# Kernel tuning notes

Measured on AMD Instinct MI355X. Metric: run time of the kernel, lower is better.

Reference implementation:

```python
import jax, jax.numpy as jnp
import numpy as np

INPUT_DIM = 1024
HIDDEN = 1024
NUM_EXPERTS = 64
TOP_K = 8
N_TOKENS = 32768


def _linear_params(key, fan_in, fan_out):
    kw, kb = jax.random.split(key)
    bound = 1.0 / np.sqrt(fan_in)
    w = jax.random.uniform(kw, (fan_in, fan_out), jnp.float32, -bound, bound)
    b = jax.random.uniform(kb, (fan_out,), jnp.float32, -bound, bound)
    return w, b


def setup_inputs() -> dict:
    key = jax.random.key(0)
    ks = jax.random.split(key, 8)
    x = jax.random.normal(ks[0], (N_TOKENS, INPUT_DIM), jnp.float32)
    noise = jax.random.normal(ks[1], (N_TOKENS, NUM_EXPERTS), jnp.float32)
    h2 = 2 * HIDDEN
    w1, b1 = _linear_params(ks[2], INPUT_DIM, h2)
    w2, b2 = _linear_params(ks[3], h2, h2)
    wn, bn = _linear_params(ks[4], h2, h2)
    w3, b3 = _linear_params(ks[5], h2, HIDDEN)
    w4, b4 = _linear_params(ks[6], HIDDEN, NUM_EXPERTS)
    wz, bz = _linear_params(ks[7], INPUT_DIM, NUM_EXPERTS)
    return {"x": x, "noise": noise, "w1": w1, "b1": b1, "w2": w2, "b2": b2,
            "wn": wn, "bn": bn, "w3": w3, "b3": b3, "w4": w4, "b4": b4,
            "wz": wz, "bz": bz}


def reference(x, noise, w1, b1, w2, b2, wn, bn, w3, b3, w4, b4, wz, bz):
    relu = jax.nn.relu
    h = relu(x @ w1 + b1)            # [N, 2H]
    h = relu(h @ w2 + b2)            # [N, 2H]
    h = relu(h @ wn + bn)            # [N, 2H]
    h = relu(h @ w3 + b3)            # [N, H]
    logits = h @ w4 + b4             # [N, E]
    noise_logits = x @ wz + bz       # [N, E]
    noisy_logits = logits + noise * jax.nn.softplus(noise_logits)
    top_k_logits, indices = jax.lax.top_k(noisy_logits, TOP_K)  # [N, K]
    rows = jnp.arange(noisy_logits.shape[0])[:, None]
    sparse_logits = jnp.full_like(noisy_logits, -jnp.inf).at[rows, indices].set(top_k_logits)
    router_output = jax.nn.softmax(sparse_logits, axis=-1)      # [N, E]
    return router_output, indices
```

## Files before the change

### kernel.cpp

```cpp
#include <hip/hip_runtime.h>
#include <math.h>

#define IN_DIM 1024
#define H2     2048
#define HID    1024
#define NEXP   64
#define TOPK   8
#define RISK_TH 1.5e-4f

typedef short  v8s __attribute__((ext_vector_type(8)));
typedef float  v4f __attribute__((ext_vector_type(4)));

__device__ __forceinline__ void bf16_split(float f, ushort& h, ushort& l) {
    unsigned uh = __float_as_uint(f) & 0xffff0000u;
    h = (ushort)(uh >> 16);
    float r = f - __uint_as_float(uh);
    l = (ushort)(__float_as_uint(r) >> 16);
}

__device__ __forceinline__ void gload16(const ushort* g, ushort* l) {
    __builtin_amdgcn_global_load_lds(
        (const __attribute__((address_space(1))) void*)g,
        (__attribute__((address_space(3))) void*)l, 16, 0, 0);
}

__global__ __launch_bounds__(256)
void split_w_kernel(const float* __restrict__ W, ushort* __restrict__ hiT,
                    ushort* __restrict__ loT, int K, int N)
{
    __shared__ float T[64][65];
    const int k0 = blockIdx.y * 64, n0 = blockIdx.x * 64;
    const int t = threadIdx.x;
#pragma unroll
    for (int j = 0; j < 4; ++j) {
        int idx = t + j * 256;
        int row = idx >> 4;
        int c4  = (idx & 15) * 4;
        float4 f = *(const float4*)(W + (long)(k0 + row) * N + n0 + c4);
        T[row][c4 + 0] = f.x; T[row][c4 + 1] = f.y;
        T[row][c4 + 2] = f.z; T[row][c4 + 3] = f.w;
    }
    __syncthreads();
#pragma unroll
    for (int j = 0; j < 4; ++j) {
        int idx = t + j * 256;
        int nn = idx >> 4;
        int kq = (idx & 15) * 4;
        ushort4 h4, l4;
        bf16_split(T[kq + 0][nn], h4.x, l4.x);
        bf16_split(T[kq + 1][nn], h4.y, l4.y);
        bf16_split(T[kq + 2][nn], h4.z, l4.z);
        bf16_split(T[kq + 3][nn], h4.w, l4.w);
        long o = (long)(n0 + nn) * K + k0 + kq;
        *(ushort4*)(hiT + o) = h4;
        *(ushort4*)(loT + o) = l4;
    }
}

__global__ __launch_bounds__(256)
void split_x_kernel(const float* __restrict__ X, ushort* __restrict__ hi,
                    ushort* __restrict__ lo)
{
    long i = ((long)blockIdx.x * 256 + threadIdx.x) * 4;
    float4 f = *(const float4*)(X + i);
    ushort4 h4, l4;
    bf16_split(f.x, h4.x, l4.x);
    bf16_split(f.y, h4.y, l4.y);
    bf16_split(f.z, h4.z, l4.z);
    bf16_split(f.w, h4.w, l4.w);
    *(ushort4*)(hi + i) = h4;
    *(ushort4*)(lo + i) = l4;
}

template<int MI, int NWN>
__global__ __launch_bounds__(512, 2)
void gemm8p_kernel(const ushort* __restrict__ gAhi, const ushort* __restrict__ gAlo,
                   const ushort* __restrict__ gBhi, const ushort* __restrict__ gBlo,
                   const float* __restrict__ bias,
                   float* __restrict__ Cf32, ushort* __restrict__ Chi,
                   ushort* __restrict__ Clo, int N, int K)
{
    static_assert(MI == 2 * NWN, "wave grid must tile 256 rows");
    constexpr int BN    = NWN * 64;
    constexpr int ATILE = 256 * 32;
    constexpr int BTILE = BN * 32;
    constexpr int BUFU  = 2 * ATILE + 2 * BTILE;
    constexpr int MH    = MI / 2;
    __shared__ __align__(16) ushort lds[2 * BUFU];

    const int tid  = threadIdx.x;
    const int w    = tid >> 6;
    const int lane = tid & 63;
    const int wm   = w / NWN;
    const int wn   = w % NWN;
    const int q    = lane >> 4;
    const int l15  = lane & 15;

    const int nwg = (int)(gridDim.x * gridDim.y);
    const int h   = (int)(blockIdx.y * gridDim.x + blockIdx.x);
    const int l   = (h & 7) * (nwg >> 3) + (h >> 3);
    const long bm = (long)(l >> 3) * 256;
    const long bn = (long)(l & 7) * BN;

    const int  e   = lane >> 2;
    const int  s8  = (((lane & 3) ^ ((lane >> 3) & 3)) * 8);
    const int  fragUS = ((q ^ ((l15 >> 1) & 3)) * 8);

    const int NT = K >> 5;

    v4f acc[MI][4];
#pragma unroll
    for (int mi = 0; mi < MI; ++mi)
#pragma unroll
        for (int ni = 0; ni < 4; ++ni)
            acc[mi][ni] = (v4f){0.f, 0.f, 0.f, 0.f};

    {
        ushort* nb = lds;
        const long grA = bm + w * 16 + e;
        gload16(gAhi + grA * K + s8,                     nb + w * 512);
        gload16(gAhi + (grA + 128) * K + s8,             nb + 128 * 32 + w * 512);
        gload16(gAlo + grA * K + s8,                     nb + ATILE + w * 512);
        gload16(gAlo + (grA + 128) * K + s8,             nb + ATILE + 128 * 32 + w * 512);
        const long grB = bn + w * 16 + e;
        gload16(gBhi + grB * K + s8,                     nb + 2 * ATILE + w * 512);
        gload16(gBlo + grB * K + s8,                     nb + 2 * ATILE + BTILE + w * 512);
        if constexpr (BN == 256) {
            gload16(gBhi + (grB + 128) * K + s8,         nb + 2 * ATILE + 128 * 32 + w * 512);
            gload16(gBlo + (grB + 128) * K + s8,         nb + 2 * ATILE + BTILE + 128 * 32 + w * 512);
        }
    }
    asm volatile("s_waitcnt vmcnt(0)" ::: "memory");
    __builtin_amdgcn_s_barrier();
    __builtin_amdgcn_sched_barrier(0);

    for (int t = 0; t < NT; ++t) {
        const ushort* cA = lds + (t & 1) * BUFU;
        const ushort* cB = cA + 2 * ATILE;
        ushort* nb = lds + ((t + 1) & 1) * BUFU;
        const bool more = (t + 1 < NT);
        const int  ktn  = (t + 1) << 5;

        v8s ah[MH], al[MH];
        v8s bh0[2], bl0[2];
        v8s bh1[2], bl1[2];

#pragma unroll
        for (int i = 0; i < MH; ++i) {
            int r = wm * (MI * 16) + i * 16 + l15;
            const ushort* pA = cA + r * 32 + fragUS;
            ah[i] = *(const v8s*)pA;
            al[i] = *(const v8s*)(pA + ATILE);
        }
#pragma unroll
        for (int j = 0; j < 2; ++j) {
            int r = wn * 64 + j * 16 + l15;
            const ushort* pB = cB + r * 32 + fragUS;
            bh0[j] = *(const v8s*)pB;
            bl0[j] = *(const v8s*)(pB + BTILE);
        }
        if (more) {
            const long gr = bm + w * 16 + e;
            gload16(gAhi + gr * K + ktn + s8,             nb + w * 512);
            gload16(gAhi + (gr + 128) * K + ktn + s8,     nb + 128 * 32 + w * 512);
            gload16(gAlo + gr * K + ktn + s8,             nb + ATILE + w * 512);
            gload16(gAlo + (gr + 128) * K + ktn + s8,     nb + ATILE + 128 * 32 + w * 512);
        }

#pragma unroll
        for (int j = 0; j < 2; ++j) {
            int r = wn * 64 + (2 + j) * 16 + l15;
            const ushort* pB = cB + r * 32 + fragUS;
            bh1[j] = *(const v8s*)pB;
            bl1[j] = *(const v8s*)(pB + BTILE);
        }

        __builtin_amdgcn_s_setprio(1);
#pragma unroll
        for (int i = 0; i < MH; ++i)
#pragma unroll
            for (int j = 0; j < 2; ++j) {
                v4f c = acc[i][j];
                c = __builtin_amdgcn_mfma_f32_16x16x32_bf16(al[i], bh0[j], c, 0, 0, 0);
                c = __builtin_amdgcn_mfma_f32_16x16x32_bf16(ah[i], bl0[j], c, 0, 0, 0);
                c = __builtin_amdgcn_mfma_f32_16x16x32_bf16(ah[i], bh0[j], c, 0, 0, 0);
                acc[i][j] = c;
            }
        __builtin_amdgcn_s_setprio(0);

        if (more) {
            const long gr = bn + w * 16 + e;
            gload16(gBhi + gr * K + ktn + s8,             nb + 2 * ATILE + w * 512);
            gload16(gBlo + gr * K + ktn + s8,             nb + 2 * ATILE + BTILE + w * 512);
            if constexpr (BN == 256) {
                gload16(gBhi + (gr + 128) * K + ktn + s8, nb + 2 * ATILE + 128 * 32 + w * 512);
                gload16(gBlo + (gr + 128) * K + ktn + s8, nb + 2 * ATILE + BTILE + 128 * 32 + w * 512);
            }
        }

        __builtin_amdgcn_s_setprio(1);
#pragma unroll
        for (int i = 0; i < MH; ++i)
#pragma unroll
            for (int j = 0; j < 2; ++j) {
                v4f c = acc[i][2 + j];
                c = __builtin_amdgcn_mfma_f32_16x16x32_bf16(al[i], bh1[j], c, 0, 0, 0);
                c = __builtin_amdgcn_mfma_f32_16x16x32_bf16(ah[i], bl1[j], c, 0, 0, 0);
                c = __builtin_amdgcn_mfma_f32_16x16x32_bf16(ah[i], bh1[j], c, 0, 0, 0);
                acc[i][2 + j] = c;
            }
        __builtin_amdgcn_s_setprio(0);

#pragma unroll
        for (int i = 0; i < MH; ++i) {
            int r = wm * (MI * 16) + (MH + i) * 16 + l15;
            const ushort* pA = cA + r * 32 + fragUS;
            ah[i] = *(const v8s*)pA;
            al[i] = *(const v8s*)(pA + ATILE);
        }

        __builtin_amdgcn_s_setprio(1);
#pragma unroll
        for (int i = 0; i < MH; ++i)
#pragma unroll
            for (int j = 0; j < 2; ++j) {
                v4f c = acc[MH + i][2 + j];
                c = __builtin_amdgcn_mfma_f32_16x16x32_bf16(al[i], bh1[j], c, 0, 0, 0);
                c = __builtin_amdgcn_mfma_f32_16x16x32_bf16(ah[i], bl1[j], c, 0, 0, 0);
                c = __builtin_amdgcn_mfma_f32_16x16x32_bf16(ah[i], bh1[j], c, 0, 0, 0);
                acc[MH + i][2 + j] = c;
            }
#pragma unroll
        for (int i = 0; i < MH; ++i)
#pragma unroll
            for (int j = 0; j < 2; ++j) {
                v4f c = acc[MH + i][j];
                c = __builtin_amdgcn_mfma_f32_16x16x32_bf16(al[i], bh0[j], c, 0, 0, 0);
                c = __builtin_amdgcn_mfma_f32_16x16x32_bf16(ah[i], bl0[j], c, 0, 0, 0);
                c = __builtin_amdgcn_mfma_f32_16x16x32_bf16(ah[i], bh0[j], c, 0, 0, 0);
                acc[MH + i][j] = c;
            }
        __builtin_amdgcn_s_setprio(0);

        asm volatile("s_waitcnt vmcnt(0)" ::: "memory");
        __builtin_amdgcn_s_barrier();
        __builtin_amdgcn_sched_barrier(0);
    }

#pragma unroll
    for (int ni = 0; ni < 4; ++ni) {
        int col = (int)(bn + wn * 64 + ni * 16 + l15);
        float bv = bias[col];
#pragma unroll
        for (int mi = 0; mi < MI; ++mi) {
            long row0 = bm + wm * (MI * 16) + mi * 16 + q * 4;
#pragma unroll
            for (int r = 0; r < 4; ++r) {
                float v = fmaxf(acc[mi][ni][r] + bv, 0.f);
                long o = (row0 + r) * (long)N + col;
                if (Cf32) {
                    Cf32[o] = v;
                } else {
                    ushort hh, ll;
                    bf16_split(v, hh, ll);
                    Chi[o] = hh;
                    Clo[o] = ll;
                }
            }
        }
    }
}

#define SBM 64
#define SBK 32
#define SLDA 68

__global__ __launch_bounds__(256, 2)
void small_gemm_kernel(const float* __restrict__ A, const float* __restrict__ B,
                       const float* __restrict__ bias, float* __restrict__ C,
                       int K)
{
    __shared__ __align__(16) float Hs[SBK][SLDA];
    __shared__ __align__(16) float Ws[SBK][NEXP];
    const int tid = threadIdx.x;
    const int tx = tid & 15;
    const int ty = tid >> 4;
    const long bm = (long)blockIdx.x * SBM;
    const float* Ab = A + bm * K;

    float acc[4][4];
#pragma unroll
    for (int i = 0; i < 4; ++i)
#pragma unroll
        for (int j = 0; j < 4; ++j) acc[i][j] = 0.f;

    float4 aR[2], bR[2];
#pragma unroll
    for (int j = 0; j < 2; ++j) {
        int idx = tid + (j << 8);
        int ar = idx >> 3, ac = (idx & 7) << 2;
        aR[j] = *(const float4*)(Ab + (long)ar * K + ac);
        int br = idx >> 4, bc = (idx & 15) << 2;
        bR[j] = *(const float4*)(B + (long)br * NEXP + bc);
    }

    int kt = 0;
    for (;;) {
#pragma unroll
        for (int j = 0; j < 2; ++j) {
            int idx = tid + (j << 8);
            int ar = idx >> 3, ac = (idx & 7) << 2;
            Hs[ac + 0][ar] = aR[j].x;
            Hs[ac + 1][ar] = aR[j].y;
            Hs[ac + 2][ar] = aR[j].z;
            Hs[ac + 3][ar] = aR[j].w;
            int br = idx >> 4, bc = (idx & 15) << 2;
            *(float4*)&Ws[br][bc] = bR[j];
        }
        __syncthreads();

        kt += SBK;
        if (kt < K) {
#pragma unroll
            for (int j = 0; j < 2; ++j) {
                int idx = tid + (j << 8);
                int ar = idx >> 3, ac = (idx & 7) << 2;
                aR[j] = *(const float4*)(Ab + (long)ar * K + kt + ac);
                int br = idx >> 4, bc = (idx & 15) << 2;
                bR[j] = *(const float4*)(B + (long)(kt + br) * NEXP + bc);
            }
        }

#pragma unroll
        for (int k = 0; k < SBK; ++k) {
            float a[4], b[4];
            *(float4*)&a[0] = *(const float4*)&Hs[k][ty * 4];
            *(float4*)&b[0] = *(const float4*)&Ws[k][tx * 4];
#pragma unroll
            for (int i = 0; i < 4; ++i)
#pragma unroll
                for (int j = 0; j < 4; ++j)
                    acc[i][j] = fmaf(a[i], b[j], acc[i][j]);
        }
        __syncthreads();
        if (kt >= K) break;
    }

    float bv[4];
#pragma unroll
    for (int j = 0; j < 4; ++j) bv[j] = bias[tx * 4 + j];
#pragma unroll
    for (int i = 0; i < 4; ++i) {
        long row = bm + ty * 4 + i;
        float o[4];
#pragma unroll
        for (int j = 0; j < 4; ++j) o[j] = acc[i][j] + bv[j];
        *(float4*)(C + row * NEXP + tx * 4) = *(const float4*)&o[0];
    }
}

__global__ __launch_bounds__(256)
void router_kernel(const float* __restrict__ logits, const float* __restrict__ nlog,
                   const float* __restrict__ noise, float* __restrict__ rout,
                   float* __restrict__ idx_out, int rows, int rowBase,
                   int* __restrict__ ctrl, int* __restrict__ list, int maxr)
{
    const int wave = threadIdx.x >> 6;
    const int lane = threadIdx.x & 63;
    const long row = (long)blockIdx.x * 4 + wave;
    if (row >= rows) return;

    float lg = logits[row * NEXP + lane];
    float nl = nlog[row * NEXP + lane];
    float nz = noise[row * NEXP + lane];
    float sp = fmaxf(nl, 0.f) + log1pf(expf(-fabsf(nl)));
    float v  = lg + nz * sp;

    float orig = v;
    float work = v;
    bool  sel  = false;
    float myidx = 0.f;
    float m = 0.f, ssum = 0.f;
    float prev = 0.f, minGap = INFINITY;

#pragma unroll
    for (int r = 0; r < TOPK + 1; ++r) {
        float bvv = work;
        int   bi  = lane;
#pragma unroll
        for (int off = 32; off > 0; off >>= 1) {
            float ov = __shfl_xor(bvv, off);
            int   oi = __shfl_xor(bi, off);
            if (ov > bvv || (ov == bvv && oi < bi)) { bvv = ov; bi = oi; }
        }
        if (r > 0) minGap = fminf(minGap, prev - bvv);
        prev = bvv;
        if (r < TOPK) {
            if (r == 0) m = bvv;
            ssum += expf(bvv - m);
            if (lane == bi) { work = -INFINITY; sel = true; }
            if (lane == r)  myidx = (float)bi;
        }
    }

    float p = sel ? expf(orig - m) / ssum : 0.f;
    rout[row * NEXP + lane] = p;
    if (lane < TOPK) idx_out[row * TOPK + lane] = myidx;

    if (lane == 0 && minGap < RISK_TH) {
        int slot = atomicAdd(ctrl, 1);
        if (slot < maxr) list[slot] = rowBase + (int)row;
    }
}

__global__ void init_kernel(int* ctrl) { if (threadIdx.x == 0) ctrl[0] = 0; }

__global__ void pad_kernel(int* ctrl, int* list, int maxr)
{
    int cnt = ctrl[0]; if (cnt > maxr) cnt = maxr;
    int rounded = (cnt + 63) & ~63; if (rounded > maxr) rounded = maxr;
    if (threadIdx.x == 0) { ctrl[1] = rounded; ctrl[2] = cnt; }
    int fill = (cnt > 0) ? list[0] : 0;
    for (int i = cnt + threadIdx.x; i < rounded; i += blockDim.x) list[i] = fill;
}

__global__ __launch_bounds__(256)
void fixzero_kernel(double* P, const float* __restrict__ bias, int cols,
                    double* Z, int zcols, const int* __restrict__ ctrl)
{
    const int rp = blockIdx.y * 64;
    if (rp >= ctrl[1]) return;
    const int c0 = blockIdx.x * 64;
    if (P && c0 < cols) {
#pragma unroll
        for (int i = 0; i < 8; ++i) {
            int idx = threadIdx.x + i * 256;
            int row = idx >> 5;
            int col = (idx & 31) * 2;
            long o = (long)(rp + row) * cols + c0 + col;
            double2 v = *(double2*)(P + o);
            v.x = fmax(v.x + (double)bias[c0 + col],     0.0);
            v.y = fmax(v.y + (double)bias[c0 + col + 1], 0.0);
            *(double2*)(P + o) = v;
        }
    }
    if (Z && c0 < zcols) {
        const double2 z2 = {0.0, 0.0};
#pragma unroll
        for (int i = 0; i < 8; ++i) {
            int idx = threadIdx.x + i * 256;
            int row = idx >> 5;
            int col = (idx & 31) * 2;
            *(double2*)(Z + (long)(rp + row) * zcols + c0 + col) = z2;
        }
    }
}

#define DBM 64
#define DBN 64
#define DBK 32

__global__ __launch_bounds__(256)
void dgemm_ks(const double* __restrict__ A64, const float* __restrict__ A32,
              const int* __restrict__ rowList,
              const float* __restrict__ B, double* __restrict__ C,
              int N, int K, int kLen, const int* __restrict__ ctrl)
{
    const int mBase = blockIdx.y * DBM;
    if (mBase >= ctrl[1]) return;
    const int kBase = blockIdx.z * kLen;
    const int kEnd  = kBase + kLen;

    __shared__ __align__(16) double As[DBM][DBK + 2];
    __shared__ __align__(16) double Bs[DBK][DBN];
    __shared__ int rowIdx[DBM];

    const int tid = threadIdx.x;
    const int tx = tid & 15;
    const int ty = tid >> 4;
    const int nBase = blockIdx.x * DBN;

    if (A32 && tid < DBM) rowIdx[tid] = rowList[mBase + tid];
    __syncthreads();

    const int ar = tid >> 4;
    const int ak = (tid & 15) * 2;
    const int bc = (tid & 15) * 4;

    int rIdx[4];
    if (A32) {
#pragma unroll
        for (int j = 0; j < 4; ++j) rIdx[j] = rowIdx[ar + j * 16];
    }

    double acc[4][4];
#pragma unroll
    for (int i = 0; i < 4; ++i)
#pragma unroll
        for (int j = 0; j < 4; ++j) acc[i][j] = 0.0;

    double2 aReg[4];
    float4  bReg[2];

    auto prefetch = [&](int ktv) {
#pragma unroll
        for (int j = 0; j < 4; ++j) {
            if (A32) {
                const float2 f = *(const float2*)(A32 + (long)rIdx[j] * K + ktv + ak);
                aReg[j].x = (double)f.x; aReg[j].y = (double)f.y;
            } else {
                aReg[j] = *(const double2*)(A64 + (long)(mBase + ar + j * 16) * K + ktv + ak);
            }
        }
#pragma unroll
        for (int j = 0; j < 2; ++j)
            bReg[j] = *(const float4*)(B + (long)(ktv + ar + j * 16) * N + nBase + bc);
    };

    prefetch(kBase);
    int kt = kBase;
    for (;;) {
#pragma unroll
        for (int j = 0; j < 4; ++j)
            *(double2*)&As[ar + j * 16][ak] = aReg[j];
#pragma unroll
        for (int j = 0; j < 2; ++j) {
            double2 lo, hi;
            lo.x = (double)bReg[j].x; lo.y = (double)bReg[j].y;
            hi.x = (double)bReg[j].z; hi.y = (double)bReg[j].w;
            *(double2*)&Bs[ar + j * 16][bc]     = lo;
            *(double2*)&Bs[ar + j * 16][bc + 2] = hi;
        }
        __syncthreads();

        kt += DBK;
        if (kt < kEnd) prefetch(kt);

#pragma unroll
        for (int k = 0; k < DBK; ++k) {
            double a[4], b[4];
#pragma unroll
            for (int i = 0; i < 4; ++i) a[i] = As[ty * 4 + i][k];
#pragma unroll
            for (int j = 0; j < 4; ++j) b[j] = Bs[k][tx + j * 16];
#pragma unroll
            for (int i = 0; i < 4; ++i)
#pragma unroll
                for (int j = 0; j < 4; ++j)
                    acc[i][j] = fma(a[i], b[j], acc[i][j]);
        }
        __syncthreads();
        if (kt >= kEnd) break;
    }

#pragma unroll
    for (int i = 0; i < 4; ++i) {
        long row = mBase + ty * 4 + i;
#pragma unroll
        for (int j = 0; j < 4; ++j) {
            int n = nBase + tx + j * 16;
#if defined(__HIP_PLATFORM_AMD__)
            unsafeAtomicAdd(&C[row * N + n], acc[i][j]);
#else
            atomicAdd(&C[row * N + n], acc[i][j]);
#endif
        }
    }
}

__global__ __launch_bounds__(256)
void router_fix_kernel(const double* __restrict__ lgd, const double* __restrict__ nld,
                       const float* __restrict__ b4f, const float* __restrict__ bzf,
                       const float* __restrict__ noise, float* __restrict__ rout,
                       float* __restrict__ idx_out,
                       const int* __restrict__ ctrl, const int* __restrict__ list)
{
    const int wave = threadIdx.x >> 6;
    const int lane = threadIdx.x & 63;
    const int i = blockIdx.x * 4 + wave;
    if (i >= ctrl[2]) return;
    const long row = list[i];

    double lg = lgd[(long)i * NEXP + lane] + (double)b4f[lane];
    double nl = nld[(long)i * NEXP + lane] + (double)bzf[lane];
    double nz = (double)noise[row * NEXP + lane];
    double sp = fmax(nl, 0.0) + log1p(exp(-fabs(nl)));
    double v  = lg + nz * sp;

    double orig = v, work = v;
    bool sel = false;
    float myidx = 0.f;
    double m = 0.0, ssum = 0.0;

#pragma unroll
    for (int r = 0; r < TOPK; ++r) {
        double bvv = work;
        int    bi  = lane;
#pragma unroll
        for (int off = 32; off > 0; off >>= 1) {
            double ov = __shfl_xor(bvv, off);
            int    oi = __shfl_xor(bi, off);
            if (ov > bvv || (ov == bvv && oi < bi)) { bvv = ov; bi = oi; }
        }
        if (r == 0) m = bvv;
        ssum += exp(bvv - m);
        if (lane == bi) { work = -INFINITY; sel = true; }
        if (lane == r)  myidx = (float)bi;
    }

    double p = sel ? exp(orig - m) / ssum : 0.0;
    rout[row * NEXP + lane] = (float)p;
    if (lane < TOPK) idx_out[row * TOPK + lane] = myidx;
}

extern "C" void kernel_launch(void* const* d_in, const int* in_sizes, int n_in,
                              void* d_out, int out_size, void* d_ws, size_t ws_size,
                              hipStream_t stream)
{
    const float* x     = (const float*)d_in[0];
    const float* noise = (const float*)d_in[1];
    const float* w1 = (const float*)d_in[2];
    const float* b1 = (const float*)d_in[3];
    const float* w2 = (const float*)d_in[4];
    const float* b2 = (const float*)d_in[5];
    const float* wn = (const float*)d_in[6];
    const float* bn = (const float*)d_in[7];
    const float* w3 = (const float*)d_in[8];
    const float* b3 = (const float*)d_in[9];
    const float* w4 = (const float*)d_in[10];
    const float* b4 = (const float*)d_in[11];
    const float* wz = (const float*)d_in[12];
    const float* bz = (const float*)d_in[13];
    float* out = (float*)d_out;

    const int Ntok = in_sizes[0] / IN_DIM;

    const size_t e1 = (size_t)IN_DIM * H2;
    const size_t e2 = (size_t)H2 * H2;
    const size_t en = (size_t)H2 * H2;
    const size_t e3 = (size_t)H2 * HID;
    size_t weightBytes = 2 * (e1 + e2 + en + e3) * sizeof(ushort);
    weightBytes = (weightBytes + 255) & ~(size_t)255;

    const size_t perTok = (size_t)4 * H2 * 2 + (size_t)IN_DIM * 4 + 2 * NEXP * 4;
    int chunk = 8192;
    while (chunk > 256) {
        size_t needb = weightBytes + (size_t)chunk * perTok + 65536;
        if (needb <= ws_size) break;
        chunk >>= 1;
    }
    if (chunk > Ntok) chunk = Ntok;

    int MAXR = chunk / 2;
    if (MAXR > 4096) MAXR = 4096;

    ushort* w1Thi = (ushort*)d_ws;
    ushort* w1Tlo = w1Thi + e1;
    ushort* w2Thi = w1Tlo + e1;
    ushort* w2Tlo = w2Thi + e2;
    ushort* wnThi = w2Tlo + e2;
    ushort* wnTlo = wnThi + en;
    ushort* w3Thi = wnTlo + en;
    ushort* w3Tlo = w3Thi + e3;

    char* region = (char*)d_ws + weightBytes;
    const size_t regionBytes = (size_t)chunk * perTok;

    ushort* pAhi = (ushort*)region;
    ushort* pAlo = pAhi + (size_t)chunk * H2;
    ushort* pBhi = pAlo + (size_t)chunk * H2;
    ushort* pBlo = pBhi + (size_t)chunk * H2;
    char*   ureg = (char*)(pBlo + (size_t)chunk * H2);
    ushort* xphi = (ushort*)ureg;
    ushort* xplo = xphi + (size_t)chunk * IN_DIM;
    float*  hfin = (float*)ureg;
    float*  lg   = (float*)(ureg + (size_t)chunk * IN_DIM * 4);
    float*  nl   = lg + (size_t)chunk * NEXP;

    double* hA  = (double*)region;
    double* hB  = hA + (size_t)MAXR * H2;
    double* lgd = hB + (size_t)MAXR * H2;
    double* nld = lgd + (size_t)MAXR * NEXP;

    int* ctrl = (int*)(region + regionBytes);
    int* list = ctrl + 16;

    float* ridx = out + (size_t)Ntok * NEXP;

    const dim3 blk(256);
    init_kernel<<<1, 64, 0, stream>>>(ctrl);

    split_w_kernel<<<dim3(H2 / 64,  IN_DIM / 64), blk, 0, stream>>>(w1, w1Thi, w1Tlo, IN_DIM, H2);
    split_w_kernel<<<dim3(H2 / 64,  H2 / 64),     blk, 0, stream>>>(w2, w2Thi, w2Tlo, H2, H2);
    split_w_kernel<<<dim3(H2 / 64,  H2 / 64),     blk, 0, stream>>>(wn, wnThi, wnTlo, H2, H2);
    split_w_kernel<<<dim3(HID / 64, H2 / 64),     blk, 0, stream>>>(w3, w3Thi, w3Tlo, H2, HID);

    for (int c0 = 0; c0 < Ntok; c0 += chunk) {
        const float* xa = x + (size_t)c0 * IN_DIM;
        split_x_kernel<<<dim3(chunk), blk, 0, stream>>>(xa, xphi, xplo);
        gemm8p_kernel<8, 4><<<dim3(H2 / 256,  chunk / 256), 512, 0, stream>>>(
            xphi, xplo, w1Thi, w1Tlo, b1, nullptr, pAhi, pAlo, H2, IN_DIM);
        gemm8p_kernel<8, 4><<<dim3(H2 / 256,  chunk / 256), 512, 0, stream>>>(
            pAhi, pAlo, w2Thi, w2Tlo, b2, nullptr, pBhi, pBlo, H2, H2);
        gemm8p_kernel<8, 4><<<dim3(H2 / 256,  chunk / 256), 512, 0, stream>>>(
            pBhi, pBlo, wnThi, wnTlo, bn, nullptr, pAhi, pAlo, H2, H2);
        gemm8p_kernel<4, 2><<<dim3(HID / 128, chunk / 256), 512, 0, stream>>>(
            pAhi, pAlo, w3Thi, w3Tlo, b3, hfin, nullptr, nullptr, HID, H2);
        small_gemm_kernel<<<dim3(chunk / SBM), blk, 0, stream>>>(hfin, w4, b4, lg, HID);
        small_gemm_kernel<<<dim3(chunk / SBM), blk, 0, stream>>>(xa,   wz, bz, nl, IN_DIM);
        router_kernel<<<dim3(chunk / 4), blk, 0, stream>>>(lg, nl, noise + (size_t)c0 * NEXP,
                                                           out + (size_t)c0 * NEXP,
                                                           ridx + (size_t)c0 * TOPK, chunk, c0,
                                                           ctrl, list, MAXR);
    }

    pad_kernel<<<1, 256, 0, stream>>>(ctrl, list, MAXR);

    const int GY = MAXR / DBM;
    fixzero_kernel<<<dim3(H2 / 64, GY), blk, 0, stream>>>(nullptr, nullptr, 0, hA, H2, ctrl);
    dgemm_ks<<<dim3(H2 / DBN, GY, 4), blk, 0, stream>>>(nullptr, x, list, w1, hA, H2, IN_DIM, IN_DIM / 4, ctrl);
    fixzero_kernel<<<dim3(H2 / 64, GY), blk, 0, stream>>>(hA, b1, H2, hB, H2, ctrl);
    dgemm_ks<<<dim3(H2 / DBN, GY, 4), blk, 0, stream>>>(hA, nullptr, nullptr, w2, hB, H2, H2, H2 / 4, ctrl);
    fixzero_kernel<<<dim3(H2 / 64, GY), blk, 0, stream>>>(hB, b2, H2, hA, H2, ctrl);
    dgemm_ks<<<dim3(H2 / DBN, GY, 4), blk, 0, stream>>>(hB, nullptr, nullptr, wn, hA, H2, H2, H2 / 4, ctrl);
    fixzero_kernel<<<dim3(H2 / 64, GY), blk, 0, stream>>>(hA, bn, H2, hB, HID, ctrl);
    dgemm_ks<<<dim3(HID / DBN, GY, 8), blk, 0, stream>>>(hA, nullptr, nullptr, w3, hB, HID, H2, H2 / 8, ctrl);
    fixzero_kernel<<<dim3(HID / 64, GY), blk, 0, stream>>>(hB, b3, HID, lgd, NEXP, ctrl);
    fixzero_kernel<<<dim3(1, GY), blk, 0, stream>>>(nullptr, nullptr, 0, nld, NEXP, ctrl);
    dgemm_ks<<<dim3(1, GY, 16), blk, 0, stream>>>(hB, nullptr, nullptr, w4, lgd, NEXP, HID, HID / 16, ctrl);
    dgemm_ks<<<dim3(1, GY, 16), blk, 0, stream>>>(nullptr, x, list, wz, nld, NEXP, IN_DIM, IN_DIM / 16, ctrl);
    router_fix_kernel<<<dim3(MAXR / 4), blk, 0, stream>>>(lgd, nld, b4, bz, noise, out, ridx, ctrl, list);
}
```

Baseline: 3.233 ms.

## Prefetch two K-tiles ahead in split-bf16 GEMM and raise fp32 fix split-K

The main bf16x3 GEMM loop now keeps two LDS tiles in flight. The next-next tile is issued after an LDS-drain barrier mid-iteration, and the end-of-iteration wait uses a partial vmcnt instead of waiting on every load. This is meant to hide global-load latency behind more MFMA work. Separately, the fp32 fix-up dgemm launches for the first three layers go from split-K 4 to 8 to add parallelism. The change adds an extra barrier per iteration, and the larger split adds more atomic or partial-sum traffic.

```diff
diff --git a/kernel.cpp b/kernel.cpp
--- a/kernel.cpp
+++ b/kernel.cpp
@@ -108,6 +108,23 @@
 
     const int NT = K >> 5;
 
+    auto stageA = [&](int ktv, ushort* nb) {
+        const long gr = bm + w * 16 + e;
+        gload16(gAhi + gr * K + ktv + s8,         nb + w * 512);
+        gload16(gAhi + (gr + 128) * K + ktv + s8, nb + 128 * 32 + w * 512);
+        gload16(gAlo + gr * K + ktv + s8,         nb + ATILE + w * 512);
+        gload16(gAlo + (gr + 128) * K + ktv + s8, nb + ATILE + 128 * 32 + w * 512);
+    };
+    auto stageB = [&](int ktv, ushort* nb) {
+        const long gr = bn + w * 16 + e;
+        gload16(gBhi + gr * K + ktv + s8,         nb + 2 * ATILE + w * 512);
+        gload16(gBlo + gr * K + ktv + s8,         nb + 2 * ATILE + BTILE + w * 512);
+        if constexpr (BN == 256) {
+            gload16(gBhi + (gr + 128) * K + ktv + s8, nb + 2 * ATILE + 128 * 32 + w * 512);
+            gload16(gBlo + (gr + 128) * K + ktv + s8, nb + 2 * ATILE + BTILE + 128 * 32 + w * 512);
+        }
+    };
+
     v4f acc[MI][4];
 #pragma unroll
     for (int mi = 0; mi < MI; ++mi)
@@ -115,31 +132,25 @@
         for (int ni = 0; ni < 4; ++ni)
             acc[mi][ni] = (v4f){0.f, 0.f, 0.f, 0.f};
 
-    {
-        ushort* nb = lds;
-        const long grA = bm + w * 16 + e;
-        gload16(gAhi + grA * K + s8,                     nb + w * 512);
-        gload16(gAhi + (grA + 128) * K + s8,             nb + 128 * 32 + w * 512);
-        gload16(gAlo + grA * K + s8,                     nb + ATILE + w * 512);
-        gload16(gAlo + (grA + 128) * K + s8,             nb + ATILE + 128 * 32 + w * 512);
-        const long grB = bn + w * 16 + e;
-        gload16(gBhi + grB * K + s8,                     nb + 2 * ATILE + w * 512);
-        gload16(gBlo + grB * K + s8,                     nb + 2 * ATILE + BTILE + w * 512);
-        if constexpr (BN == 256) {
-            gload16(gBhi + (grB + 128) * K + s8,         nb + 2 * ATILE + 128 * 32 + w * 512);
-            gload16(gBlo + (grB + 128) * K + s8,         nb + 2 * ATILE + BTILE + 128 * 32 + w * 512);
-        }
-    }
-    asm volatile("s_waitcnt vmcnt(0)" ::: "memory");
+    stageA(0, lds);
+    stageB(0, lds);
+    if (NT > 1) {
+        stageA(32, lds + BUFU);
+        stageB(32, lds + BUFU);
+        if constexpr (BN == 256) asm volatile("s_waitcnt vmcnt(8)" ::: "memory");
+        else                     asm volatile("s_waitcnt vmcnt(6)" ::: "memory");
+    } else {
+        asm volatile("s_waitcnt vmcnt(0)" ::: "memory");
+    }
     __builtin_amdgcn_s_barrier();
     __builtin_amdgcn_sched_barrier(0);
 
     for (int t = 0; t < NT; ++t) {
         const ushort* cA = lds + (t & 1) * BUFU;
         const ushort* cB = cA + 2 * ATILE;
-        ushort* nb = lds + ((t + 1) & 1) * BUFU;
-        const bool more = (t + 1 < NT);
-        const int  ktn  = (t + 1) << 5;
+        ushort* rb = lds + (t & 1) * BUFU;
+        const bool issue2 = (t + 2 < NT);
+        const int  kt2 = (t + 2) << 5;
 
         v8s ah[MH], al[MH];
         v8s bh0[2], bl0[2];
@@ -159,14 +170,6 @@
             bh0[j] = *(const v8s*)pB;
             bl0[j] = *(const v8s*)(pB + BTILE);
         }
-        if (more) {
-            const long gr = bm + w * 16 + e;
-            gload16(gAhi + gr * K + ktn + s8,             nb + w * 512);
-            gload16(gAhi + (gr + 128) * K + ktn + s8,     nb + 128 * 32 + w * 512);
-            gload16(gAlo + gr * K + ktn + s8,             nb + ATILE + w * 512);
-            gload16(gAlo + (gr + 128) * K + ktn + s8,     nb + ATILE + 128 * 32 + w * 512);
-        }
-
 #pragma unroll
         for (int j = 0; j < 2; ++j) {
             int r = wn * 64 + (2 + j) * 16 + l15;
@@ -188,16 +191,6 @@
             }
         __builtin_amdgcn_s_setprio(0);
 
-        if (more) {
-            const long gr = bn + w * 16 + e;
-            gload16(gBhi + gr * K + ktn + s8,             nb + 2 * ATILE + w * 512);
-            gload16(gBlo + gr * K + ktn + s8,             nb + 2 * ATILE + BTILE + w * 512);
-            if constexpr (BN == 256) {
-                gload16(gBhi + (gr + 128) * K + ktn + s8, nb + 2 * ATILE + 128 * 32 + w * 512);
-                gload16(gBlo + (gr + 128) * K + ktn + s8, nb + 2 * ATILE + BTILE + 128 * 32 + w * 512);
-            }
-        }
-
         __builtin_amdgcn_s_setprio(1);
 #pragma unroll
         for (int i = 0; i < MH; ++i)
@@ -218,6 +211,15 @@
             ah[i] = *(const v8s*)pA;
             al[i] = *(const v8s*)(pA + ATILE);
         }
+        asm volatile("s_waitcnt lgkmcnt(0)" ::: "memory");
+        __builtin_amdgcn_sched_barrier(0);
+        __builtin_amdgcn_s_barrier();
+        __builtin_amdgcn_sched_barrier(0);
+        if (issue2) {
+            stageA(kt2, rb);
+            stageB(kt2, rb);
+        }
+        __builtin_amdgcn_sched_barrier(0);
 
         __builtin_amdgcn_s_setprio(1);
 #pragma unroll
@@ -242,9 +244,17 @@
             }
         __builtin_amdgcn_s_setprio(0);
 
-        asm volatile("s_waitcnt vmcnt(0)" ::: "memory");
-        __builtin_amdgcn_s_barrier();
-        __builtin_amdgcn_sched_barrier(0);
+        if (t + 1 < NT) {
+            if (issue2) {
+                if constexpr (BN == 256) asm volatile("s_waitcnt vmcnt(8)" ::: "memory");
+                else                     asm volatile("s_waitcnt vmcnt(6)" ::: "memory");
+            } else {
+                asm volatile("s_waitcnt vmcnt(0)" ::: "memory");
+            }
+            __builtin_amdgcn_sched_barrier(0);
+            __builtin_amdgcn_s_barrier();
+            __builtin_amdgcn_sched_barrier(0);
+        }
     }
 
 #pragma unroll
@@ -718,11 +728,11 @@
 
     const int GY = MAXR / DBM;
     fixzero_kernel<<<dim3(H2 / 64, GY), blk, 0, stream>>>(nullptr, nullptr, 0, hA, H2, ctrl);
-    dgemm_ks<<<dim3(H2 / DBN, GY, 4), blk, 0, stream>>>(nullptr, x, list, w1, hA, H2, IN_DIM, IN_DIM / 4, ctrl);
+    dgemm_ks<<<dim3(H2 / DBN, GY, 8), blk, 0, stream>>>(nullptr, x, list, w1, hA, H2, IN_DIM, IN_DIM / 8, ctrl);
     fixzero_kernel<<<dim3(H2 / 64, GY), blk, 0, stream>>>(hA, b1, H2, hB, H2, ctrl);
-    dgemm_ks<<<dim3(H2 / DBN, GY, 4), blk, 0, stream>>>(hA, nullptr, nullptr, w2, hB, H2, H2, H2 / 4, ctrl);
+    dgemm_ks<<<dim3(H2 / DBN, GY, 8), blk, 0, stream>>>(hA, nullptr, nullptr, w2, hB, H2, H2, H2 / 8, ctrl);
     fixzero_kernel<<<dim3(H2 / 64, GY), blk, 0, stream>>>(hB, b2, H2, hA, H2, ctrl);
-    dgemm_ks<<<dim3(H2 / DBN, GY, 4), blk, 0, stream>>>(hB, nullptr, nullptr, wn, hA, H2, H2, H2 / 4, ctrl);
+    dgemm_ks<<<dim3(H2 / DBN, GY, 8), blk, 0, stream>>>(hB, nullptr, nullptr, wn, hA, H2, H2, H2 / 8, ctrl);
     fixzero_kernel<<<dim3(H2 / 64, GY), blk, 0, stream>>>(hA, bn, H2, hB, HID, ctrl);
     dgemm_ks<<<dim3(HID / DBN, GY, 8), blk, 0, stream>>>(hA, nullptr, nullptr, w3, hB, HID, H2, H2 / 8, ctrl);
     fixzero_kernel<<<dim3(HID / 64, GY), blk, 0, stream>>>(hB, b3, HID, lgd, NEXP, ctrl);
```

Measured after the change: 3.167 ms. 2.0% less time.
